# Optimization experiments

Hardware: AMD Instinct MI355X
Metric: run time of the kernel (lower is better)

Reference implementation:

```python
import jax, jax.numpy as jnp
import numpy as np

NEG_RATIO = 5.0
EPS = 1e-8
B, T = 512, 32768


def setup_inputs() -> dict:
    key = jax.random.key(0)
    k1, k2 = jax.random.split(key, 2)
    pred = jax.random.uniform(k1, (B, T), dtype=jnp.float32)      # probabilities in [0,1)
    target = jax.random.randint(k2, (B, T), 0, 8, dtype=jnp.int32)
    mask = jnp.ones((B, T), dtype=jnp.float32)
    return {"pred": pred, "target": target, "mask": mask}


def reference(pred, target, mask):
    # as the module is designed for).
    t = (target == 0).astype(pred.dtype)

    # F.binary_cross_entropy clamps log terms at -100.
    log_p = jnp.maximum(jnp.log(pred), -100.0)
    log_1mp = jnp.maximum(jnp.log1p(-pred), -100.0)
    loss = -(t * log_p + (1.0 - t) * log_1mp)

    loss = loss * mask
    t = t * mask

    pos = (t == 1.0).astype(pred.dtype)
    neg = (t == 0.0).astype(pred.dtype)
    pos_count = jnp.sum(pos)
    neg_count_all = jnp.sum(neg)
    # int(pos_count * 5.0) is exact for integer pos_count and ratio 5.0
    neg_count = jnp.minimum(neg_count_all, pos_count * NEG_RATIO)

    pos_loss = jnp.sum(loss * pos)

    # top-k over flattened negative losses with data-dependent k, done
    # jit-compatibly: full descending sort + rank mask.
    neg_sorted = jnp.sort((loss * neg).reshape(-1))[::-1]
    ranks = jnp.arange(neg_sorted.shape[0], dtype=pred.dtype)
    take = (ranks < neg_count).astype(pred.dtype)
    neg_loss = jnp.sum(neg_sorted * take)

    balance = (pos_loss + neg_loss) / (pos_count + neg_count + EPS)
    # pred==0 positives fallback: mean over all (masked) losses
    return jnp.where(pos_count == 0.0, jnp.mean(loss), balance)
```

## Files before the change

### kernel.cpp

```cpp
#include <hip/hip_runtime.h>

#define NBLK 1024
#define NTHR 256
#define H1_BINS 2048
#define H1_SHIFT 20
#define H2_BINS (1u << H1_SHIFT)
#define H2_MASK (H2_BINS - 1u)
#define CHUNK 2048
#define NCHUNK 512
#define UNROLL 4
#define TILE (NTHR * UNROLL)

#define OFF_CNT   1024
#define OFF_SUM   17408
#define OFF_P1    40960
#define OFF_CCNT  57344
#define OFF_CW    61440
#define OFF_H2    65536
#define MEMSET1   33792

#define LN2F 0.69314718055994531f
#define FIXSCALE 8388608.0f
#define INV_FIX  (1.0 / 8388608.0)
#define CNT_SHIFT 44
#define SUM_MASK ((1ULL << CNT_SHIFT) - 1ULL)
#define APPROX_GATE 3e-3

__device__ __forceinline__ void elem_compute(float pp, int tt, float mm,
                                             float& loss, bool& pos, bool& neg) {
    bool isz = (tt == 0);
    float x = isz ? pp : (1.0f - pp);
    float lr = fminf(-__log2f(x) * LN2F, 100.0f);
    loss = lr * mm;
    float tm = isz ? mm : 0.0f;
    pos = (tm == 1.0f);
    neg = (tm == 0.0f);
}

__global__ __launch_bounds__(NTHR) void pass1(const float* __restrict__ pred,
                                              const int* __restrict__ targ,
                                              const float* __restrict__ mask,
                                              int n,
                                              unsigned long long* __restrict__ gcnt,
                                              unsigned long long* __restrict__ gsum,
                                              unsigned long long* __restrict__ ctrl,
                                              double* __restrict__ p1part) {
    __shared__ unsigned long long spack[H1_BINS];
    __shared__ double sredd[NTHR];
    __shared__ unsigned sredu[NTHR];
    int tid = threadIdx.x;
    for (int i = tid; i < H1_BINS; i += NTHR) spack[i] = 0ULL;
    __syncthreads();

    float posLoss = 0.f, totLoss = 0.f;
    unsigned posCnt = 0, negCnt = 0;

    int nv = n >> 2;
    const float4* p4 = (const float4*)pred;
    const int4*   t4 = (const int4*)targ;
    const float4* m4 = (const float4*)mask;

    int tiles = (nv + TILE - 1) / TILE;
    int perblk = (tiles + NBLK - 1) / NBLK;
    int tstart = blockIdx.x * perblk;
    int tend = tstart + perblk; if (tend > tiles) tend = tiles;

    for (int tt = tstart; tt < tend; ++tt) {
        int g = tt * TILE + tid;
        bool full = (tt * TILE + TILE) <= nv;
        float4 p[UNROLL]; int4 t[UNROLL]; float4 m[UNROLL];
        bool ok[UNROLL];
        if (full) {
            #pragma unroll
            for (int k = 0; k < UNROLL; ++k) {
                p[k] = p4[g + k * NTHR]; t[k] = t4[g + k * NTHR]; m[k] = m4[g + k * NTHR];
                ok[k] = true;
            }
        } else {
            #pragma unroll
            for (int k = 0; k < UNROLL; ++k) {
                ok[k] = (g + k * NTHR) < nv;
                if (ok[k]) { p[k] = p4[g + k * NTHR]; t[k] = t4[g + k * NTHR]; m[k] = m4[g + k * NTHR]; }
            }
        }
        #pragma unroll
        for (int k = 0; k < UNROLL; ++k) {
            if (!ok[k]) continue;
            float pa[4] = {p[k].x, p[k].y, p[k].z, p[k].w};
            int   ta[4] = {t[k].x, t[k].y, t[k].z, t[k].w};
            float ma[4] = {m[k].x, m[k].y, m[k].z, m[k].w};
            #pragma unroll
            for (int j = 0; j < 4; ++j) {
                float loss; bool pos, neg;
                elem_compute(pa[j], ta[j], ma[j], loss, pos, neg);
                totLoss += loss;
                if (pos) { posCnt++; posLoss += loss; }
                if (neg) {
                    negCnt++;
                    unsigned u = __float_as_uint(loss);
                    if (u & 0x80000000u) u = 0u;
                    unsigned long long pk = (1ULL << CNT_SHIFT) |
                                            (unsigned long long)(loss * FIXSCALE);
                    atomicAdd(&spack[u >> H1_SHIFT], pk);
                }
            }
        }
    }
    for (int i = (nv << 2) + blockIdx.x * blockDim.x + tid; i < n; i += gridDim.x * blockDim.x) {
        float loss; bool pos, neg;
        elem_compute(pred[i], targ[i], mask[i], loss, pos, neg);
        totLoss += loss;
        if (pos) { posCnt++; posLoss += loss; }
        if (neg) {
            negCnt++;
            unsigned u = __float_as_uint(loss);
            if (u & 0x80000000u) u = 0u;
            unsigned long long pk = (1ULL << CNT_SHIFT) |
                                    (unsigned long long)(loss * FIXSCALE);
            atomicAdd(&spack[u >> H1_SHIFT], pk);
        }
    }
    __syncthreads();
    for (int b = tid; b < H1_BINS; b += NTHR) {
        unsigned long long pk = spack[b];
        if (pk) {
            atomicAdd(&gcnt[b], pk >> CNT_SHIFT);
            atomicAdd(&gsum[b], pk & SUM_MASK);
        }
    }
    sredd[tid] = (double)posLoss; __syncthreads();
    for (int s = NTHR / 2; s > 0; s >>= 1) { if (tid < s) sredd[tid] += sredd[tid + s]; __syncthreads(); }
    if (tid == 0) p1part[2 * blockIdx.x] = sredd[0];
    __syncthreads();
    sredd[tid] = (double)totLoss; __syncthreads();
    for (int s = NTHR / 2; s > 0; s >>= 1) { if (tid < s) sredd[tid] += sredd[tid + s]; __syncthreads(); }
    if (tid == 0) p1part[2 * blockIdx.x + 1] = sredd[0];
    __syncthreads();
    sredu[tid] = posCnt; __syncthreads();
    for (int s = NTHR / 2; s > 0; s >>= 1) { if (tid < s) sredu[tid] += sredu[tid + s]; __syncthreads(); }
    if (tid == 0) atomicAdd(&ctrl[0], (unsigned long long)sredu[0]);
    __syncthreads();
    sredu[tid] = negCnt; __syncthreads();
    for (int s = NTHR / 2; s > 0; s >>= 1) { if (tid < s) sredu[tid] += sredu[tid + s]; __syncthreads(); }
    if (tid == 0) atomicAdd(&ctrl[1], (unsigned long long)sredu[0]);
}

__global__ __launch_bounds__(1024) void findbin(const unsigned long long* __restrict__ gcnt,
                                                const unsigned long long* __restrict__ gsum,
                                                unsigned long long* __restrict__ ctrl,
                                                const double* __restrict__ p1part) {
    __shared__ double sd[1024];
    __shared__ unsigned long long ssA[1024];
    __shared__ unsigned long long ssB[1024];
    int tid = threadIdx.x;
    sd[tid] = p1part[2 * tid]; __syncthreads();
    for (int s = 512; s > 0; s >>= 1) { if (tid < s) sd[tid] += sd[tid + s]; __syncthreads(); }
    double posLoss = sd[0]; __syncthreads();
    sd[tid] = p1part[2 * tid + 1]; __syncthreads();
    for (int s = 512; s > 0; s >>= 1) { if (tid < s) sd[tid] += sd[tid + s]; __syncthreads(); }
    double totLoss = sd[0]; __syncthreads();

    unsigned long long posCnt = ctrl[0];
    unsigned long long negCnt = ctrl[1];
    unsigned long long k = posCnt * 5ULL;
    if (k > negCnt) k = negCnt;

    int base = tid * 2;
    unsigned long long h0 = gcnt[base], h1 = gcnt[base + 1];
    unsigned long long f0 = gsum[base], f1 = gsum[base + 1];
    ssA[tid] = h0 + h1; ssB[tid] = f0 + f1; __syncthreads();
    for (int d = 1; d < 1024; d <<= 1) {
        unsigned long long a = (tid + d < 1024) ? ssA[tid + d] : 0ULL;
        unsigned long long b = (tid + d < 1024) ? ssB[tid + d] : 0ULL;
        __syncthreads();
        ssA[tid] += a; ssB[tid] += b;
        __syncthreads();
    }
    unsigned long long run  = (tid == 1023) ? 0ULL : ssA[tid + 1];
    unsigned long long frun = (tid == 1023) ? 0ULL : ssB[tid + 1];

    if (k > 0) {
        unsigned long long hh[2] = {h1, h0};
        unsigned long long ff[2] = {f1, f0};
        int off[2] = {1, 0};
        #pragma unroll
        for (int j = 0; j < 2; ++j) {
            unsigned long long c = hh[j];
            if (run < k && k <= run + c) {
                unsigned b1 = (unsigned)(base + off[j]);
                unsigned long long need = k - run;
                double sumAbove = (double)frun * INV_FIX;
                double avg = ((double)ff[j] / (double)c) * INV_FIX;
                double approxWithin = (double)need * avg;
                int e = (int)((b1 >> 3) & 0xFF);
                double width = ldexp(1.0, (e > 0 ? e : 1) - 130);
                double denom = (double)posCnt + (double)k + 1e-8;
                double errBound = (double)need * width / denom;
                ctrl[2] = (unsigned long long)b1;
                ctrl[3] = need;
                ((double*)ctrl)[7] = sumAbove;
                ((double*)ctrl)[8] = approxWithin;
                ctrl[9] = (errBound <= APPROX_GATE) ? 1ULL : 0ULL;
            }
            run += c; frun += ff[j];
        }
    } else if (tid == 0) {
        ctrl[2] = (unsigned long long)H1_BINS;
        ctrl[3] = 0;
        ((double*)ctrl)[7] = 0.0;
        ((double*)ctrl)[8] = 0.0;
        ctrl[9] = 1ULL;
    }
    if (tid == 0) {
        ctrl[4] = k;
        ((double*)ctrl)[5] = posLoss;
        ((double*)ctrl)[6] = totLoss;
    }
}

__global__ __launch_bounds__(NTHR) void pass2x(const float* __restrict__ pred,
                                               const int* __restrict__ targ,
                                               const float* __restrict__ mask,
                                               int n,
                                               const unsigned long long* __restrict__ ctrl,
                                               unsigned* __restrict__ gH2) {
    if (ctrl[9] == 1ULL) return;
    unsigned b1 = (unsigned)ctrl[2];
    int tid = threadIdx.x;
    int nv = n >> 2;
    const float4* p4 = (const float4*)pred;
    const int4*   t4 = (const int4*)targ;
    const float4* m4 = (const float4*)mask;

    int tiles = (nv + TILE - 1) / TILE;
    int perblk = (tiles + NBLK - 1) / NBLK;
    int tstart = blockIdx.x * perblk;
    int tend = tstart + perblk; if (tend > tiles) tend = tiles;

    for (int tt = tstart; tt < tend; ++tt) {
        int g = tt * TILE + tid;
        bool full = (tt * TILE + TILE) <= nv;
        float4 p[UNROLL]; int4 t[UNROLL]; float4 m[UNROLL];
        bool ok[UNROLL];
        if (full) {
            #pragma unroll
            for (int k = 0; k < UNROLL; ++k) {
                p[k] = p4[g + k * NTHR]; t[k] = t4[g + k * NTHR]; m[k] = m4[g + k * NTHR];
                ok[k] = true;
            }
        } else {
            #pragma unroll
            for (int k = 0; k < UNROLL; ++k) {
                ok[k] = (g + k * NTHR) < nv;
                if (ok[k]) { p[k] = p4[g + k * NTHR]; t[k] = t4[g + k * NTHR]; m[k] = m4[g + k * NTHR]; }
            }
        }
        #pragma unroll
        for (int k = 0; k < UNROLL; ++k) {
            if (!ok[k]) continue;
            float pa[4] = {p[k].x, p[k].y, p[k].z, p[k].w};
            int   ta[4] = {t[k].x, t[k].y, t[k].z, t[k].w};
            float ma[4] = {m[k].x, m[k].y, m[k].z, m[k].w};
            #pragma unroll
            for (int j = 0; j < 4; ++j) {
                float loss; bool pos, neg;
                elem_compute(pa[j], ta[j], ma[j], loss, pos, neg);
                if (neg) {
                    unsigned u = __float_as_uint(loss);
                    if (u & 0x80000000u) u = 0u;
                    if ((u >> H1_SHIFT) == b1) atomicAdd(&gH2[u & H2_MASK], 1u);
                }
            }
        }
    }
    for (int i = (nv << 2) + blockIdx.x * blockDim.x + tid; i < n; i += gridDim.x * blockDim.x) {
        float loss; bool pos, neg;
        elem_compute(pred[i], targ[i], mask[i], loss, pos, neg);
        if (neg) {
            unsigned u = __float_as_uint(loss);
            if (u & 0x80000000u) u = 0u;
            if ((u >> H1_SHIFT) == b1) atomicAdd(&gH2[u & H2_MASK], 1u);
        }
    }
}

__global__ __launch_bounds__(256) void chunkscan(const unsigned* __restrict__ gH2,
                                                 const unsigned long long* __restrict__ ctrl,
                                                 unsigned long long* __restrict__ chunkCnt,
                                                 double* __restrict__ chunkW) {
    __shared__ unsigned long long sc[256];
    __shared__ double sw[256];
    int tid = threadIdx.x;
    unsigned b1 = (unsigned)ctrl[2];
    bool active = (ctrl[9] == 0ULL) && (b1 < H1_BINS);
    int base = blockIdx.x * CHUNK;
    unsigned long long cnt = 0; double w = 0.0;
    if (active) {
        for (int i = tid; i < CHUNK; i += 256) {
            unsigned c = gH2[base + i];
            if (c) {
                float L = __uint_as_float((b1 << H1_SHIFT) | (unsigned)(base + i));
                cnt += c;
                w += (double)c * (double)L;
            }
        }
    }
    sc[tid] = cnt; sw[tid] = w; __syncthreads();
    for (int s = 128; s > 0; s >>= 1) {
        if (tid < s) { sc[tid] += sc[tid + s]; sw[tid] += sw[tid + s]; }
        __syncthreads();
    }
    if (tid == 0) { chunkCnt[blockIdx.x] = sc[0]; chunkW[blockIdx.x] = sw[0]; }
}

__global__ __launch_bounds__(512) void finalize(const unsigned* __restrict__ gH2,
                                                const unsigned long long* __restrict__ ctrl,
                                                const unsigned long long* __restrict__ chunkCnt,
                                                const double* __restrict__ chunkW,
                                                float* __restrict__ out, int n) {
    __shared__ unsigned long long sc[512];
    __shared__ double sw[512];
    __shared__ int s_cstar;
    __shared__ unsigned long long s_rem;
    __shared__ double s_wAbove;
    __shared__ double s_res;
    int tid = threadIdx.x;

    unsigned long long posCnt = ctrl[0];
    unsigned long long b1 = ctrl[2];
    unsigned long long need = ctrl[3];
    unsigned long long k = ctrl[4];
    double posLoss = ((const double*)ctrl)[5];
    double totLoss = ((const double*)ctrl)[6];
    double sumAbove = ((const double*)ctrl)[7];
    double approxWithin = ((const double*)ctrl)[8];
    unsigned long long mode = ctrl[9];

    double within = approxWithin;

    if (mode == 0ULL && need > 0) {
        if (tid == 0) { s_cstar = 0; s_rem = 1; s_wAbove = 0.0; s_res = 0.0; }
        unsigned long long myc = chunkCnt[tid];
        double myw = chunkW[tid];
        sc[tid] = myc; sw[tid] = myw; __syncthreads();
        for (int d = 1; d < 512; d <<= 1) {
            unsigned long long ac = (tid + d < 512) ? sc[tid + d] : 0ULL;
            double aw = (tid + d < 512) ? sw[tid + d] : 0.0;
            __syncthreads();
            sc[tid] += ac; sw[tid] += aw;
            __syncthreads();
        }
        unsigned long long afterC = (tid == 511) ? 0ULL : sc[tid + 1];
        double afterW = (tid == 511) ? 0.0 : sw[tid + 1];
        if (afterC < need && need <= afterC + myc) {
            s_cstar = tid; s_rem = need - afterC; s_wAbove = afterW;
        }
        __syncthreads();
        int cstar = s_cstar;
        unsigned long long rem = s_rem;
        double wAbove = s_wAbove;
        __syncthreads();

        int pb = cstar * CHUNK + 4 * tid;
        unsigned c[4]; double L[4];
        unsigned long long tot = 0; double wtot = 0.0;
        #pragma unroll
        for (int j = 0; j < 4; ++j) {
            c[j] = gH2[pb + j];
            L[j] = (double)__uint_as_float(((unsigned)b1 << H1_SHIFT) | (unsigned)(pb + j));
            tot += c[j];
            wtot += (double)c[j] * L[j];
        }
        sc[tid] = tot; sw[tid] = wtot;
        __syncthreads();
        for (int d = 1; d < 512; d <<= 1) {
            unsigned long long ac = (tid + d < 512) ? sc[tid + d] : 0ULL;
            double aw = (tid + d < 512) ? sw[tid + d] : 0.0;
            __syncthreads();
            sc[tid] += ac; sw[tid] += aw;
            __syncthreads();
        }
        unsigned long long run = (tid == 511) ? 0ULL : sc[tid + 1];
        double wrun = (tid == 511) ? 0.0 : sw[tid + 1];
        #pragma unroll
        for (int j = 3; j >= 0; --j) {
            if (run < rem && rem <= run + c[j]) {
                s_res = wrun + (double)(rem - run) * L[j];
            }
            run += c[j];
            wrun += (double)c[j] * L[j];
        }
        __syncthreads();
        within = wAbove + s_res;
    }

    if (tid == 0) {
        double negLoss = sumAbove + within;
        double result;
        if (posCnt == 0) {
            result = totLoss / (double)n;
        } else {
            result = (posLoss + negLoss) / ((double)posCnt + (double)k + 1e-8);
        }
        out[0] = (float)result;
    }
}

extern "C" void kernel_launch(void* const* d_in, const int* in_sizes, int n_in,
                              void* d_out, int out_size, void* d_ws, size_t ws_size,
                              hipStream_t stream) {
    const float* pred = (const float*)d_in[0];
    const int*   targ = (const int*)d_in[1];
    const float* mask = (const float*)d_in[2];
    int n = in_sizes[0];

    char* ws = (char*)d_ws;
    unsigned long long* ctrl = (unsigned long long*)ws;
    unsigned long long* gcnt = (unsigned long long*)(ws + OFF_CNT);
    unsigned long long* gsum = (unsigned long long*)(ws + OFF_SUM);
    double* p1part = (double*)(ws + OFF_P1);
    unsigned long long* chunkCnt = (unsigned long long*)(ws + OFF_CCNT);
    double* chunkW = (double*)(ws + OFF_CW);
    unsigned* gH2 = (unsigned*)(ws + OFF_H2);

    (void)hipMemsetAsync(ws, 0, MEMSET1, stream);
    (void)hipMemsetAsync(ws + OFF_H2, 0, H2_BINS * 4, stream);

    pass1<<<NBLK, NTHR, 0, stream>>>(pred, targ, mask, n, gcnt, gsum, ctrl, p1part);
    findbin<<<1, 1024, 0, stream>>>(gcnt, gsum, ctrl, p1part);
    pass2x<<<NBLK, NTHR, 0, stream>>>(pred, targ, mask, n, ctrl, gH2);
    chunkscan<<<NCHUNK, 256, 0, stream>>>(gH2, ctrl, chunkCnt, chunkW);
    finalize<<<1, 512, 0, stream>>>(gH2, ctrl, chunkCnt, chunkW, (float*)d_out, n);
}
```

Measured before the change: 71.67 us.

## Double-buffer pass1 input loads through LDS with async global_load_lds

Replaces pass1's direct float4 register loads with asynchronous global-to-LDS copies into double buffers, prefetching the next 1024-element stage while the current one is processed, and synchronizing with explicit vmcnt/lgkmcnt waits. It also lowers the grid from 1024 to 768 blocks, widens the packed count shift so per-block sums have more headroom, and guards the findbin reduction for the smaller block count. The aim is to hide memory latency. In exchange, the unroll depth drops to one float4 per input per thread per stage, and correctness depends on the hand-written waitcnt ordering.

```diff
diff --git a/kernel.cpp b/kernel.cpp
--- a/kernel.cpp
+++ b/kernel.cpp
@@ -1,6 +1,6 @@
 #include <hip/hip_runtime.h>
 
-#define NBLK 1024
+#define NBLK 768
 #define NTHR 256
 #define H1_BINS 2048
 #define H1_SHIFT 20
@@ -10,6 +10,7 @@
 #define NCHUNK 512
 #define UNROLL 4
 #define TILE (NTHR * UNROLL)
+#define STAGE_ELEMS 1024
 
 #define OFF_CNT   1024
 #define OFF_SUM   17408
@@ -22,9 +23,13 @@
 #define LN2F 0.69314718055994531f
 #define FIXSCALE 8388608.0f
 #define INV_FIX  (1.0 / 8388608.0)
-#define CNT_SHIFT 44
+#define CNT_SHIFT 46
 #define SUM_MASK ((1ULL << CNT_SHIFT) - 1ULL)
 #define APPROX_GATE 3e-3
+
+#define WAIT_VM3()   asm volatile("s_waitcnt vmcnt(3)" ::: "memory")
+#define WAIT_VM0()   asm volatile("s_waitcnt vmcnt(0)" ::: "memory")
+#define WAIT_LGKM0() asm volatile("s_waitcnt lgkmcnt(0)" ::: "memory")
 
 __device__ __forceinline__ void elem_compute(float pp, int tt, float mm,
                                              float& loss, bool& pos, bool& neg) {
@@ -37,6 +42,13 @@
     neg = (tm == 0.0f);
 }
 
+__device__ __forceinline__ void stage16(const void* g, void* l) {
+    __builtin_amdgcn_global_load_lds(
+        (const __attribute__((address_space(1))) unsigned int*)g,
+        (__attribute__((address_space(3))) unsigned int*)l,
+        16, 0, 0);
+}
+
 __global__ __launch_bounds__(NTHR) void pass1(const float* __restrict__ pred,
                                               const int* __restrict__ targ,
                                               const float* __restrict__ mask,
@@ -45,50 +57,52 @@
                                               unsigned long long* __restrict__ gsum,
                                               unsigned long long* __restrict__ ctrl,
                                               double* __restrict__ p1part) {
+    __shared__ unsigned char sbufP[2][4096];
+    __shared__ unsigned char sbufT[2][4096];
+    __shared__ unsigned char sbufM[2][4096];
     __shared__ unsigned long long spack[H1_BINS];
     __shared__ double sredd[NTHR];
     __shared__ unsigned sredu[NTHR];
     int tid = threadIdx.x;
+    int w = tid >> 6;
+    int wbase = w << 10;
     for (int i = tid; i < H1_BINS; i += NTHR) spack[i] = 0ULL;
     __syncthreads();
 
     float posLoss = 0.f, totLoss = 0.f;
     unsigned posCnt = 0, negCnt = 0;
 
-    int nv = n >> 2;
-    const float4* p4 = (const float4*)pred;
-    const int4*   t4 = (const int4*)targ;
-    const float4* m4 = (const float4*)mask;
-
-    int tiles = (nv + TILE - 1) / TILE;
-    int perblk = (tiles + NBLK - 1) / NBLK;
-    int tstart = blockIdx.x * perblk;
-    int tend = tstart + perblk; if (tend > tiles) tend = tiles;
-
-    for (int tt = tstart; tt < tend; ++tt) {
-        int g = tt * TILE + tid;
-        bool full = (tt * TILE + TILE) <= nv;
-        float4 p[UNROLL]; int4 t[UNROLL]; float4 m[UNROLL];
-        bool ok[UNROLL];
-        if (full) {
-            #pragma unroll
-            for (int k = 0; k < UNROLL; ++k) {
-                p[k] = p4[g + k * NTHR]; t[k] = t4[g + k * NTHR]; m[k] = m4[g + k * NTHR];
-                ok[k] = true;
-            }
-        } else {
-            #pragma unroll
-            for (int k = 0; k < UNROLL; ++k) {
-                ok[k] = (g + k * NTHR) < nv;
-                if (ok[k]) { p[k] = p4[g + k * NTHR]; t[k] = t4[g + k * NTHR]; m[k] = m4[g + k * NTHR]; }
-            }
-        }
-        #pragma unroll
-        for (int k = 0; k < UNROLL; ++k) {
-            if (!ok[k]) continue;
-            float pa[4] = {p[k].x, p[k].y, p[k].z, p[k].w};
-            int   ta[4] = {t[k].x, t[k].y, t[k].z, t[k].w};
-            float ma[4] = {m[k].x, m[k].y, m[k].z, m[k].w};
+    int totStages = n >> 10;
+    int perblk = (totStages + NBLK - 1) / NBLK;
+    int sBeg = blockIdx.x * perblk;
+    int sEnd = sBeg + perblk; if (sEnd > totStages) sEnd = totStages;
+
+    if (sBeg < sEnd) {
+        {
+            int e = (sBeg << 10) + tid * 4;
+            stage16(pred + e, &sbufP[0][wbase]);
+            stage16(targ + e, &sbufT[0][wbase]);
+            stage16(mask + e, &sbufM[0][wbase]);
+        }
+        int b = 0;
+        for (int s = sBeg; s < sEnd; ++s) {
+            bool more = (s + 1 < sEnd);
+            if (more) {
+                int e = ((s + 1) << 10) + tid * 4;
+                stage16(pred + e, &sbufP[b ^ 1][wbase]);
+                stage16(targ + e, &sbufT[b ^ 1][wbase]);
+                stage16(mask + e, &sbufM[b ^ 1][wbase]);
+                WAIT_VM3();
+            } else {
+                WAIT_VM0();
+            }
+            float4 p = *(const float4*)&sbufP[b][tid * 16];
+            int4   t = *(const int4*)  &sbufT[b][tid * 16];
+            float4 m = *(const float4*)&sbufM[b][tid * 16];
+            WAIT_LGKM0();
+            float pa[4] = {p.x, p.y, p.z, p.w};
+            int   ta[4] = {t.x, t.y, t.z, t.w};
+            float ma[4] = {m.x, m.y, m.z, m.w};
             #pragma unroll
             for (int j = 0; j < 4; ++j) {
                 float loss; bool pos, neg;
@@ -104,9 +118,11 @@
                     atomicAdd(&spack[u >> H1_SHIFT], pk);
                 }
             }
-        }
-    }
-    for (int i = (nv << 2) + blockIdx.x * blockDim.x + tid; i < n; i += gridDim.x * blockDim.x) {
+            b ^= 1;
+        }
+    }
+    for (int i = (totStages << 10) + blockIdx.x * blockDim.x + tid; i < n;
+         i += gridDim.x * blockDim.x) {
         float loss; bool pos, neg;
         elem_compute(pred[i], targ[i], mask[i], loss, pos, neg);
         totLoss += loss;
@@ -121,11 +137,11 @@
         }
     }
     __syncthreads();
-    for (int b = tid; b < H1_BINS; b += NTHR) {
-        unsigned long long pk = spack[b];
+    for (int bidx = tid; bidx < H1_BINS; bidx += NTHR) {
+        unsigned long long pk = spack[bidx];
         if (pk) {
-            atomicAdd(&gcnt[b], pk >> CNT_SHIFT);
-            atomicAdd(&gsum[b], pk & SUM_MASK);
+            atomicAdd(&gcnt[bidx], pk >> CNT_SHIFT);
+            atomicAdd(&gsum[bidx], pk & SUM_MASK);
         }
     }
     sredd[tid] = (double)posLoss; __syncthreads();
@@ -153,10 +169,10 @@
     __shared__ unsigned long long ssA[1024];
     __shared__ unsigned long long ssB[1024];
     int tid = threadIdx.x;
-    sd[tid] = p1part[2 * tid]; __syncthreads();
+    sd[tid] = (tid < NBLK) ? p1part[2 * tid] : 0.0; __syncthreads();
     for (int s = 512; s > 0; s >>= 1) { if (tid < s) sd[tid] += sd[tid + s]; __syncthreads(); }
     double posLoss = sd[0]; __syncthreads();
-    sd[tid] = p1part[2 * tid + 1]; __syncthreads();
+    sd[tid] = (tid < NBLK) ? p1part[2 * tid + 1] : 0.0; __syncthreads();
     for (int s = 512; s > 0; s >>= 1) { if (tid < s) sd[tid] += sd[tid + s]; __syncthreads(); }
     double totLoss = sd[0]; __syncthreads();
 
```

Result: slower. 75.29 us (+5.1%).
